# Kernel tuning notes

Measured on AMD Instinct MI355X. Metric: run time of the kernel, lower is better.

Reference implementation:

```python
import jax, jax.numpy as jnp
import numpy as np

N_NODES = 100000
N_EDGES = 1600000
N_FEAT = 128
N_HID = 128
N_CLS = 40
DROP_P = 0.5


def setup_inputs() -> dict:
    key = jax.random.key(0)
    k1, k2, k3, k4 = jax.random.split(key, 4)
    x = jax.random.normal(k1, (N_NODES, N_FEAT), dtype=jnp.float32)
    edge_index = jax.random.randint(k2, (2, N_EDGES), 0, N_NODES, dtype=jnp.int32)
    W1 = jax.random.normal(k3, (N_FEAT, N_HID), dtype=jnp.float32) / np.sqrt(N_FEAT)
    b1 = jnp.zeros((N_HID,), dtype=jnp.float32)
    W2 = jax.random.normal(k4, (N_HID, N_CLS), dtype=jnp.float32) / np.sqrt(N_HID)
    b2 = jnp.zeros((N_CLS,), dtype=jnp.float32)
    return {"x": x, "edge_index": edge_index, "W1": W1, "b1": b1, "W2": W2, "b2": b2}


def _gcn_norm(edge_index, num_nodes):
    # add self-loops, then symmetric normalization D^-1/2 (A+I) D^-1/2
    loops = jnp.arange(num_nodes, dtype=edge_index.dtype)
    src = jnp.concatenate([edge_index[0], loops])
    dst = jnp.concatenate([edge_index[1], loops])
    deg = jax.ops.segment_sum(jnp.ones_like(dst, dtype=jnp.float32), dst,
                              num_segments=num_nodes)
    deg_isqrt = jax.lax.rsqrt(deg)  # deg >= 1 thanks to self-loops
    norm = deg_isqrt[src] * deg_isqrt[dst]  # [E+N]
    return src, dst, norm


def _gcn_conv(x, src, dst, norm, W, b, num_nodes):
    h = x @ W                                   # [N, out]
    msg = h[src] * norm[:, None]                # gather + scale, [E+N, out]
    out = jax.ops.segment_sum(msg, dst, num_segments=num_nodes)  # scatter-add
    return out + b


def reference(x, edge_index, W1, b1, W2, b2):
    num_nodes = x.shape[0]
    src, dst, norm = _gcn_norm(edge_index, num_nodes)
    h = _gcn_conv(x, src, dst, norm, W1, b1, num_nodes)
    h = jax.nn.relu(h)
    # dropout(p=0.5, training=True) with a fixed key for determinism
    keep = jax.random.uniform(jax.random.key(42), h.shape) >= DROP_P
    h = jnp.where(keep, h / (1.0 - DROP_P), 0.0)
    out = _gcn_conv(h, src, dst, norm, W2, b2, num_nodes)
    return out
```

## Files before the change

kernel.cpp:

```cpp
#include <hip/hip_runtime.h>

#define N_NODES 100000
#define N_EDGES 1600000
#define NBUCK 196
#define G1B 3125
#define FB 391
#define FEDGE 4096
#define BCAP 9216

__device__ __forceinline__ unsigned pack_bf16(float a, float b){
  unsigned ua = __float_as_uint(a), ub = __float_as_uint(b);
  ua = ua + 0x7fffu + ((ua >> 16) & 1u);
  ub = ub + 0x7fffu + ((ub >> 16) & 1u);
  return (ua >> 16) | (ub & 0xffff0000u);
}
__device__ __forceinline__ unsigned short bf16_of(float a){
  unsigned ua = __float_as_uint(a);
  ua = ua + 0x7fffu + ((ua >> 16) & 1u);
  return (unsigned short)(ua >> 16);
}
__device__ __forceinline__ float bf_lo(unsigned u){ return __uint_as_float(u << 16); }
__device__ __forceinline__ float bf_hi(unsigned u){ return __uint_as_float(u & 0xffff0000u); }

__device__ __forceinline__ unsigned tf_rotl(unsigned x, int r){ return (x<<r)|(x>>(32-r)); }

__device__ __forceinline__ unsigned dropout_keep(unsigned e){
  unsigned x0 = 0u, x1 = e;
  const unsigned k0 = 0u, k1v = 42u;
  const unsigned k2 = 0x1BD11BDAu ^ k0 ^ k1v;
#define TF_R(r) { x0 += x1; x1 = tf_rotl(x1,(r)); x1 ^= x0; }
  x0 += k0; x1 += k1v;
  TF_R(13) TF_R(15) TF_R(26) TF_R(6)
  x0 += k1v; x1 += k2 + 1u;
  TF_R(17) TF_R(29) TF_R(16) TF_R(24)
  x0 += k2; x1 += k0 + 2u;
  TF_R(13) TF_R(15) TF_R(26) TF_R(6)
  x0 += k0; x1 += k1v + 3u;
  TF_R(17) TF_R(29) TF_R(16) TF_R(24)
  x0 += k1v; x1 += k2 + 4u;
  TF_R(13) TF_R(15) TF_R(26) TF_R(6)
  x0 += k2; x1 += k0 + 5u;
#undef TF_R
  return (x0 ^ x1) >> 31;
}

__device__ __forceinline__ void gemm1_block(int gb, int t, float* smem,
                                            const float* __restrict__ x,
                                            const float* __restrict__ W1,
                                            unsigned* __restrict__ h1g){
  float* xs = smem;
  float* Wq = smem + 4096;
  size_t row0 = (size_t)gb * 32;

  const float4* xv = (const float4*)(x + row0*128);
  float4* xsv = (float4*)xs;
  #pragma unroll
  for (int j = 0; j < 4; j++) xsv[t + 256*j] = xv[t + 256*j];

  int tx = t & 31, ty = t >> 5;
  float acc[4][4] = {};
  const float4* Wv = (const float4*)W1;
  float4* Wqv = (float4*)Wq;
  const float* xr = xs + (ty*4)*128;

  for (int q = 0; q < 4; q++){
    __syncthreads();
    #pragma unroll
    for (int j = 0; j < 4; j++) Wqv[t + 256*j] = Wv[q*1024 + t + 256*j];
    __syncthreads();
    int kbase = q*32;
    #pragma unroll 8
    for (int kk = 0; kk < 32; kk++){
      float4 w = *(const float4*)(Wq + kk*128 + tx*4);
      int k = kbase + kk;
      float x0 = xr[k], x1 = xr[128 + k], x2 = xr[256 + k], x3 = xr[384 + k];
      acc[0][0] = fmaf(x0, w.x, acc[0][0]); acc[0][1] = fmaf(x0, w.y, acc[0][1]);
      acc[0][2] = fmaf(x0, w.z, acc[0][2]); acc[0][3] = fmaf(x0, w.w, acc[0][3]);
      acc[1][0] = fmaf(x1, w.x, acc[1][0]); acc[1][1] = fmaf(x1, w.y, acc[1][1]);
      acc[1][2] = fmaf(x1, w.z, acc[1][2]); acc[1][3] = fmaf(x1, w.w, acc[1][3]);
      acc[2][0] = fmaf(x2, w.x, acc[2][0]); acc[2][1] = fmaf(x2, w.y, acc[2][1]);
      acc[2][2] = fmaf(x2, w.z, acc[2][2]); acc[2][3] = fmaf(x2, w.w, acc[2][3]);
      acc[3][0] = fmaf(x3, w.x, acc[3][0]); acc[3][1] = fmaf(x3, w.y, acc[3][1]);
      acc[3][2] = fmaf(x3, w.z, acc[3][2]); acc[3][3] = fmaf(x3, w.w, acc[3][3]);
    }
  }
  #pragma unroll
  for (int i = 0; i < 4; i++){
    uint2 o;
    o.x = pack_bf16(acc[i][0], acc[i][1]);
    o.y = pack_bf16(acc[i][2], acc[i][3]);
    *(uint2*)(h1g + (row0 + ty*4 + i)*64 + tx*2) = o;
  }
}

__launch_bounds__(256)
__global__ void k_B(const float* __restrict__ x, const float* __restrict__ W1,
                    unsigned* __restrict__ h1g,
                    const int* __restrict__ src, const int* __restrict__ dst,
                    int* __restrict__ bcur2, int2* __restrict__ tmp, int N, int E){
  extern __shared__ float smem[];
  int t = threadIdx.x;
  if (blockIdx.x < FB){
    int* hist = (int*)smem;
    int fb = blockIdx.x;
    for (int i = t; i < NBUCK; i += 256) hist[i] = 0;
    __syncthreads();
    int e0 = fb*FEDGE;
    #pragma unroll 4
    for (int j = 0; j < FEDGE/256; j++){
      int e = e0 + t + j*256;
      if (e < E) atomicAdd(&hist[dst[e] >> 9], 1);
    }
    __syncthreads();
    if (t < NBUCK){
      int c = hist[t];
      if (c > 0) hist[t] = t*BCAP + atomicAdd(&bcur2[t], c);
    }
    __syncthreads();
    #pragma unroll 4
    for (int j = 0; j < FEDGE/256; j++){
      int e = e0 + t + j*256;
      if (e < E){
        int d = dst[e], s = src[e];
        int p = atomicAdd(&hist[d >> 9], 1);
        tmp[p] = make_int2(s, d);
      }
    }
    return;
  }
  int gb = blockIdx.x - FB;
  if (gb < G1B) gemm1_block(gb, t, smem, x, W1, h1g);
}

__launch_bounds__(512)
__global__ void k_hist(const int2* __restrict__ tmp, const int* __restrict__ bcur2,
                       int* __restrict__ degi, int* __restrict__ off,
                       float* __restrict__ dii, int N){
  __shared__ int cur[512];
  __shared__ int wtot[8];
  int b = blockIdx.x, t = threadIdx.x;
  cur[t] = 0;
  __syncthreads();
  int m = bcur2[b];
  int base = b*BCAP;
  int node0 = b << 9;
  for (int i = t; i < m; i += 512)
    atomicAdd(&cur[tmp[base + i].y - node0], 1);
  __syncthreads();
  int v = cur[t];
  int lane = t & 63, w = t >> 6;
  int incl = v;
  for (int d = 1; d < 64; d <<= 1){
    int y = __shfl_up(incl, d);
    if (lane >= d) incl += y;
  }
  if (lane == 63) wtot[w] = incl;
  __syncthreads();
  int wb = 0;
  for (int i = 0; i < w; i++) wb += wtot[i];
  int excl = wb + incl - v;
  int n = node0 + t;
  if (n < N){
    degi[n] = v;
    off[n]  = base + excl;
    dii[n]  = rsqrtf((float)(v + 1));
  }
}

__launch_bounds__(1024)
__global__ void k_csort(const int2* __restrict__ tmp, int2* __restrict__ csre,
                        const int* __restrict__ off, const int* __restrict__ bcur2,
                        const float* __restrict__ dii, int N){
  __shared__ int   cur[512];
  __shared__ float dl[512];
  int b = blockIdx.x, t = threadIdx.x;
  int node0 = b << 9;
  if (t < 512){
    int n = node0 + t;
    cur[t] = (n < N) ? off[n] : 0;
    dl[t]  = (n < N) ? dii[n] : 0.f;
  }
  __syncthreads();
  int m = bcur2[b];
  int base = b*BCAP;
  for (int i = t; i < m; i += 1024){
    int2 r = tmp[base + i];
    int dloc = r.y - node0;
    float w = dii[r.x] * dl[dloc];
    int p = atomicAdd(&cur[dloc], 1);
    csre[p] = make_int2(r.x, __float_as_int(w));
  }
}

__launch_bounds__(256)
__global__ void k_agg1(const unsigned* __restrict__ h1g, unsigned* __restrict__ Bbg,
                       const int2* __restrict__ csre, const int* __restrict__ off,
                       const int* __restrict__ degi, const float* __restrict__ dii,
                       const float* __restrict__ b1, int N){
  int n = blockIdx.x*4 + (threadIdx.x >> 6);
  int lane = threadIdx.x & 63;
  if (n >= N) return;
  n = __builtin_amdgcn_readfirstlane(n);
  float din = dii[n];
  float s2 = din*din;
  unsigned su = h1g[(size_t)n*64 + lane];
  float a0 = bf_lo(su)*s2, a1 = bf_hi(su)*s2;
  int o = off[n], cnt = degi[n];
  int i = 0;
  for (; i + 8 <= cnt; i += 8){
    int2 e0 = csre[o+i+0], e1 = csre[o+i+1], e2 = csre[o+i+2], e3 = csre[o+i+3];
    int2 e4 = csre[o+i+4], e5 = csre[o+i+5], e6 = csre[o+i+6], e7 = csre[o+i+7];
    unsigned u0 = h1g[(size_t)e0.x*64 + lane];
    unsigned u1 = h1g[(size_t)e1.x*64 + lane];
    unsigned u2 = h1g[(size_t)e2.x*64 + lane];
    unsigned u3 = h1g[(size_t)e3.x*64 + lane];
    unsigned u4 = h1g[(size_t)e4.x*64 + lane];
    unsigned u5 = h1g[(size_t)e5.x*64 + lane];
    unsigned u6 = h1g[(size_t)e6.x*64 + lane];
    unsigned u7 = h1g[(size_t)e7.x*64 + lane];
    float w0 = __int_as_float(e0.y), w1 = __int_as_float(e1.y);
    float w2 = __int_as_float(e2.y), w3 = __int_as_float(e3.y);
    float w4 = __int_as_float(e4.y), w5 = __int_as_float(e5.y);
    float w6 = __int_as_float(e6.y), w7 = __int_as_float(e7.y);
    a0 = fmaf(bf_lo(u0), w0, a0); a1 = fmaf(bf_hi(u0), w0, a1);
    a0 = fmaf(bf_lo(u1), w1, a0); a1 = fmaf(bf_hi(u1), w1, a1);
    a0 = fmaf(bf_lo(u2), w2, a0); a1 = fmaf(bf_hi(u2), w2, a1);
    a0 = fmaf(bf_lo(u3), w3, a0); a1 = fmaf(bf_hi(u3), w3, a1);
    a0 = fmaf(bf_lo(u4), w4, a0); a1 = fmaf(bf_hi(u4), w4, a1);
    a0 = fmaf(bf_lo(u5), w5, a0); a1 = fmaf(bf_hi(u5), w5, a1);
    a0 = fmaf(bf_lo(u6), w6, a0); a1 = fmaf(bf_hi(u6), w6, a1);
    a0 = fmaf(bf_lo(u7), w7, a0); a1 = fmaf(bf_hi(u7), w7, a1);
  }
  for (; i < cnt; ++i){
    int2 e = csre[o+i];
    unsigned u = h1g[(size_t)e.x*64 + lane];
    float w = __int_as_float(e.y);
    a0 = fmaf(bf_lo(u), w, a0); a1 = fmaf(bf_hi(u), w, a1);
  }
  float2 bb = *(const float2*)(b1 + lane*2);
  a0 = fmaxf(a0 + bb.x, 0.f);
  a1 = fmaxf(a1 + bb.y, 0.f);
  unsigned e0i = (unsigned)n*128u + (unsigned)lane*2u;
  a0 = dropout_keep(e0i)      ? a0*2.f : 0.f;
  a1 = dropout_keep(e0i + 1u) ? a1*2.f : 0.f;
  Bbg[(size_t)n*64 + lane] = pack_bf16(a0, a1);
}

__launch_bounds__(256)
__global__ void k_gemm2(const unsigned* __restrict__ Bbg, const float* __restrict__ W2,
                        unsigned short* __restrict__ h2p, int N){
  __shared__ float W2T[40*132];
  __shared__ float Bs[64*132];
  int t = threadIdx.x;
  int row0 = blockIdx.x * 64;
  for (int idx = t; idx < 128*40; idx += 256){
    int r = idx / 40, c = idx - 40*r;
    W2T[c*132 + r] = W2[idx];
  }
  #pragma unroll
  for (int j = 0; j < 8; j++){
    int idx = t + 256*j;
    int r = idx >> 5, c2 = idx & 31;
    int gr = row0 + r; if (gr > N-1) gr = N-1;
    uint2 v = *(const uint2*)(Bbg + (size_t)gr*64 + c2*2);
    float4 f = { bf_lo(v.x), bf_hi(v.x), bf_lo(v.y), bf_hi(v.y) };
    *(float4*)(Bs + r*132 + c2*4) = f;
  }
  __syncthreads();

  int cg = t & 7, rg = t >> 3;
  int c0 = cg*5, r0 = rg*2;
  float acc[2][5] = {};
  #pragma unroll 4
  for (int k = 0; k < 128; k++){
    float bv0 = Bs[r0*132 + k], bv1 = Bs[(r0+1)*132 + k];
    #pragma unroll
    for (int u = 0; u < 5; u++){
      float w = W2T[(c0+u)*132 + k];
      acc[0][u] = fmaf(bv0, w, acc[0][u]);
      acc[1][u] = fmaf(bv1, w, acc[1][u]);
    }
  }
  #pragma unroll
  for (int i = 0; i < 2; i++){
    int gr = row0 + r0 + i;
    if (gr < N){
      #pragma unroll
      for (int u = 0; u < 5; u++) h2p[(size_t)gr*64 + c0 + u] = bf16_of(acc[i][u]);
    }
  }
}

__launch_bounds__(256)
__global__ void k_agg2(const unsigned* __restrict__ h2p, float* __restrict__ out,
                       const int2* __restrict__ csre, const int* __restrict__ off,
                       const int* __restrict__ degi, const float* __restrict__ dii,
                       const float* __restrict__ b2, int N){
  int n = blockIdx.x*4 + (threadIdx.x >> 6);
  int lane31 = threadIdx.x & 31;
  int lane   = threadIdx.x & 63;
  if (n >= N) return;
  n = __builtin_amdgcn_readfirstlane(n);
  float din = dii[n];
  float s2 = din*din;
  unsigned su = h2p[(size_t)n*32 + lane31];
  float a0 = bf_lo(su)*s2, a1 = bf_hi(su)*s2;
  int o = off[n], cnt = degi[n];
  int i = 0;
  for (; i + 8 <= cnt; i += 8){
    int2 e0 = csre[o+i+0], e1 = csre[o+i+1], e2 = csre[o+i+2], e3 = csre[o+i+3];
    int2 e4 = csre[o+i+4], e5 = csre[o+i+5], e6 = csre[o+i+6], e7 = csre[o+i+7];
    unsigned u0 = h2p[(size_t)e0.x*32 + lane31];
    unsigned u1 = h2p[(size_t)e1.x*32 + lane31];
    unsigned u2 = h2p[(size_t)e2.x*32 + lane31];
    unsigned u3 = h2p[(size_t)e3.x*32 + lane31];
    unsigned u4 = h2p[(size_t)e4.x*32 + lane31];
    unsigned u5 = h2p[(size_t)e5.x*32 + lane31];
    unsigned u6 = h2p[(size_t)e6.x*32 + lane31];
    unsigned u7 = h2p[(size_t)e7.x*32 + lane31];
    float w0 = __int_as_float(e0.y), w1 = __int_as_float(e1.y);
    float w2 = __int_as_float(e2.y), w3 = __int_as_float(e3.y);
    float w4 = __int_as_float(e4.y), w5 = __int_as_float(e5.y);
    float w6 = __int_as_float(e6.y), w7 = __int_as_float(e7.y);
    a0 = fmaf(bf_lo(u0), w0, a0); a1 = fmaf(bf_hi(u0), w0, a1);
    a0 = fmaf(bf_lo(u1), w1, a0); a1 = fmaf(bf_hi(u1), w1, a1);
    a0 = fmaf(bf_lo(u2), w2, a0); a1 = fmaf(bf_hi(u2), w2, a1);
    a0 = fmaf(bf_lo(u3), w3, a0); a1 = fmaf(bf_hi(u3), w3, a1);
    a0 = fmaf(bf_lo(u4), w4, a0); a1 = fmaf(bf_hi(u4), w4, a1);
    a0 = fmaf(bf_lo(u5), w5, a0); a1 = fmaf(bf_hi(u5), w5, a1);
    a0 = fmaf(bf_lo(u6), w6, a0); a1 = fmaf(bf_hi(u6), w6, a1);
    a0 = fmaf(bf_lo(u7), w7, a0); a1 = fmaf(bf_hi(u7), w7, a1);
  }
  for (; i < cnt; ++i){
    int2 e = csre[o+i];
    unsigned u = h2p[(size_t)e.x*32 + lane31];
    float w = __int_as_float(e.y);
    a0 = fmaf(bf_lo(u), w, a0); a1 = fmaf(bf_hi(u), w, a1);
  }
  if (lane < 20){
    float2 bb = *(const float2*)(b2 + lane*2);
    a0 += bb.x;
    a1 += bb.y;
    *(float2*)(out + (size_t)n*40 + lane*2) = make_float2(a0, a1);
  }
}

extern "C" void kernel_launch(void* const* d_in, const int* in_sizes, int n_in,
                              void* d_out, int out_size, void* d_ws, size_t ws_size,
                              hipStream_t stream){
  const float* x  = (const float*)d_in[0];
  const int*   ei = (const int*)  d_in[1];
  const float* W1 = (const float*)d_in[2];
  const float* b1 = (const float*)d_in[3];
  const float* W2 = (const float*)d_in[4];
  const float* b2 = (const float*)d_in[5];
  float* out = (float*)d_out;
  char* ws = (char*)d_ws;
  const int N = N_NODES, E = N_EDGES;
  const int* srcv = ei;
  const int* dstv = ei + E;

  int*   bcur2 = (int*)  (ws + 0);
  int*   off   = (int*)  (ws + 8192);
  int*   degi  = (int*)  (ws + 417792);
  float* dii   = (float*)(ws + 827392);
  int2*  tmp   = (int2*) (ws + 1236992);
  int2*  csre  = (int2*) (ws + 15687680);
  unsigned*       h1g = (unsigned*)      (ws + 30138368);
  unsigned short* h2p = (unsigned short*)(ws + 30138368);
  unsigned*       Bbg = (unsigned*)      (ws + 55738368);

  hipMemsetAsync(bcur2, 0, 8192, stream);

  k_B<<<FB + G1B, 256, 32768, stream>>>(x, W1, h1g, srcv, dstv, bcur2, tmp, N, E);
  k_hist<<<NBUCK, 512, 0, stream>>>(tmp, bcur2, degi, off, dii, N);
  k_csort<<<NBUCK, 1024, 0, stream>>>(tmp, csre, off, bcur2, dii, N);

  k_agg1 <<<N/4, 256, 0, stream>>>(h1g, Bbg, csre, off, degi, dii, b1, N);
  k_gemm2<<<(N + 63)/64, 256, 0, stream>>>(Bbg, W2, h2p, N);
  k_agg2 <<<N/4, 256, 0, stream>>>((const unsigned*)h2p, out, csre, off, degi, dii, b2, N);
}
```

Measured before the change: 242.2 us.

## Compute first-layer GEMM with bf16 MFMA using pre-transposed bf16 W1

Replaces the fp32 shared-memory FMA GEMM for x@W1 with a register-fed bf16 MFMA 16x16x32 kernel. A small extra kernel first transposes W1 and converts it to bf16, and each wave then loads its x rows directly from global memory and converts them to bf16. Shared memory is no longer used, so the fused graph-bucketing blocks run with less LDS, but it adds a launch. x is now rounded to bf16 before the multiply, and the output stores are scalar 16-bit writes.

Result: faster. 229.7 us (-5.1%).

```diff
diff --git a/kernel.cpp b/kernel.cpp
--- a/kernel.cpp
+++ b/kernel.cpp
@@ -3,10 +3,13 @@
 #define N_NODES 100000
 #define N_EDGES 1600000
 #define NBUCK 196
-#define G1B 3125
+#define G1B 1563
 #define FB 391
 #define FEDGE 4096
 #define BCAP 9216
+
+typedef __attribute__((ext_vector_type(8))) short short8v;
+typedef __attribute__((ext_vector_type(4))) float f32x4;
 
 __device__ __forceinline__ unsigned pack_bf16(float a, float b){
   unsigned ua = __float_as_uint(a), ub = __float_as_uint(b);
@@ -44,64 +47,20 @@
   return (x0 ^ x1) >> 31;
 }
 
-__device__ __forceinline__ void gemm1_block(int gb, int t, float* smem,
-                                            const float* __restrict__ x,
-                                            const float* __restrict__ W1,
-                                            unsigned* __restrict__ h1g){
-  float* xs = smem;
-  float* Wq = smem + 4096;
-  size_t row0 = (size_t)gb * 32;
-
-  const float4* xv = (const float4*)(x + row0*128);
-  float4* xsv = (float4*)xs;
-  #pragma unroll
-  for (int j = 0; j < 4; j++) xsv[t + 256*j] = xv[t + 256*j];
-
-  int tx = t & 31, ty = t >> 5;
-  float acc[4][4] = {};
-  const float4* Wv = (const float4*)W1;
-  float4* Wqv = (float4*)Wq;
-  const float* xr = xs + (ty*4)*128;
-
-  for (int q = 0; q < 4; q++){
-    __syncthreads();
-    #pragma unroll
-    for (int j = 0; j < 4; j++) Wqv[t + 256*j] = Wv[q*1024 + t + 256*j];
-    __syncthreads();
-    int kbase = q*32;
-    #pragma unroll 8
-    for (int kk = 0; kk < 32; kk++){
-      float4 w = *(const float4*)(Wq + kk*128 + tx*4);
-      int k = kbase + kk;
-      float x0 = xr[k], x1 = xr[128 + k], x2 = xr[256 + k], x3 = xr[384 + k];
-      acc[0][0] = fmaf(x0, w.x, acc[0][0]); acc[0][1] = fmaf(x0, w.y, acc[0][1]);
-      acc[0][2] = fmaf(x0, w.z, acc[0][2]); acc[0][3] = fmaf(x0, w.w, acc[0][3]);
-      acc[1][0] = fmaf(x1, w.x, acc[1][0]); acc[1][1] = fmaf(x1, w.y, acc[1][1]);
-      acc[1][2] = fmaf(x1, w.z, acc[1][2]); acc[1][3] = fmaf(x1, w.w, acc[1][3]);
-      acc[2][0] = fmaf(x2, w.x, acc[2][0]); acc[2][1] = fmaf(x2, w.y, acc[2][1]);
-      acc[2][2] = fmaf(x2, w.z, acc[2][2]); acc[2][3] = fmaf(x2, w.w, acc[2][3]);
-      acc[3][0] = fmaf(x3, w.x, acc[3][0]); acc[3][1] = fmaf(x3, w.y, acc[3][1]);
-      acc[3][2] = fmaf(x3, w.z, acc[3][2]); acc[3][3] = fmaf(x3, w.w, acc[3][3]);
-    }
-  }
-  #pragma unroll
-  for (int i = 0; i < 4; i++){
-    uint2 o;
-    o.x = pack_bf16(acc[i][0], acc[i][1]);
-    o.y = pack_bf16(acc[i][2], acc[i][3]);
-    *(uint2*)(h1g + (row0 + ty*4 + i)*64 + tx*2) = o;
-  }
+__global__ void k_wt(const float* __restrict__ W1, unsigned short* __restrict__ W1T){
+  int idx = blockIdx.x*256 + threadIdx.x;
+  int k = idx >> 7, n = idx & 127;
+  W1T[n*128 + k] = bf16_of(W1[idx]);
 }
 
 __launch_bounds__(256)
-__global__ void k_B(const float* __restrict__ x, const float* __restrict__ W1,
-                    unsigned* __restrict__ h1g,
+__global__ void k_B(const float* __restrict__ x, const unsigned short* __restrict__ W1T,
+                    unsigned short* __restrict__ h1u,
                     const int* __restrict__ src, const int* __restrict__ dst,
                     int* __restrict__ bcur2, int2* __restrict__ tmp, int N, int E){
-  extern __shared__ float smem[];
+  __shared__ int hist[NBUCK];
   int t = threadIdx.x;
   if (blockIdx.x < FB){
-    int* hist = (int*)smem;
     int fb = blockIdx.x;
     for (int i = t; i < NBUCK; i += 256) hist[i] = 0;
     __syncthreads();
@@ -129,7 +88,44 @@
     return;
   }
   int gb = blockIdx.x - FB;
-  if (gb < G1B) gemm1_block(gb, t, smem, x, W1, h1g);
+  if (gb >= G1B) return;
+  int w = t >> 6, l = t & 63;
+  int lo = l & 15, hi = l >> 4;
+  int rowA = gb*64 + w*16 + lo;
+  int rA = (rowA < N) ? rowA : (N-1);
+  const float4* xr = (const float4*)(x + (size_t)rA*128);
+
+  short8v a[4];
+  #pragma unroll
+  for (int kk = 0; kk < 4; kk++){
+    float4 f0 = xr[kk*8 + 2*hi];
+    float4 f1 = xr[kk*8 + 2*hi + 1];
+    union { short8v v; unsigned u[4]; } A;
+    A.u[0] = pack_bf16(f0.x, f0.y);
+    A.u[1] = pack_bf16(f0.z, f0.w);
+    A.u[2] = pack_bf16(f1.x, f1.y);
+    A.u[3] = pack_bf16(f1.z, f1.w);
+    a[kk] = A.v;
+  }
+  int rowC0 = gb*64 + w*16 + hi*4;
+  #pragma unroll
+  for (int tt = 0; tt < 8; tt++){
+    int n0 = tt*16;
+    const uint4* brow = (const uint4*)(W1T + (n0 + lo)*128);
+    f32x4 acc = {0.f, 0.f, 0.f, 0.f};
+    #pragma unroll
+    for (int kk = 0; kk < 4; kk++){
+      union { short8v v; uint4 q; } B;
+      B.q = brow[kk*4 + hi];
+      acc = __builtin_amdgcn_mfma_f32_16x16x32_bf16(a[kk], B.v, acc, 0, 0, 0);
+    }
+    int colC = n0 + lo;
+    #pragma unroll
+    for (int r = 0; r < 4; r++){
+      int rc = rowC0 + r;
+      if (rc < N) h1u[(size_t)rc*128 + colC] = bf16_of(acc[r]);
+    }
+  }
 }
 
 __launch_bounds__(512)
@@ -364,15 +360,18 @@
   int*   off   = (int*)  (ws + 8192);
   int*   degi  = (int*)  (ws + 417792);
   float* dii   = (float*)(ws + 827392);
-  int2*  tmp   = (int2*) (ws + 1236992);
-  int2*  csre  = (int2*) (ws + 15687680);
-  unsigned*       h1g = (unsigned*)      (ws + 30138368);
-  unsigned short* h2p = (unsigned short*)(ws + 30138368);
-  unsigned*       Bbg = (unsigned*)      (ws + 55738368);
+  unsigned short* W1T = (unsigned short*)(ws + 1236992);
+  int2*  tmp   = (int2*) (ws + 1269760);
+  int2*  csre  = (int2*) (ws + 15720448);
+  unsigned short* h1u = (unsigned short*)(ws + 30171136);
+  unsigned*       h1g = (unsigned*)      (ws + 30171136);
+  unsigned short* h2p = (unsigned short*)(ws + 30171136);
+  unsigned*       Bbg = (unsigned*)      (ws + 55771136);
 
   hipMemsetAsync(bcur2, 0, 8192, stream);
-
-  k_B<<<FB + G1B, 256, 32768, stream>>>(x, W1, h1g, srcv, dstv, bcur2, tmp, N, E);
+  k_wt<<<64, 256, 0, stream>>>(W1, W1T);
+
+  k_B<<<FB + G1B, 256, 0, stream>>>(x, W1T, h1u, srcv, dstv, bcur2, tmp, N, E);
   k_hist<<<NBUCK, 512, 0, stream>>>(tmp, bcur2, degi, off, dii, N);
   k_csort<<<NBUCK, 1024, 0, stream>>>(tmp, csre, off, bcur2, dii, N);
 
```
